# Performance work log

Measured on AMD Instinct MI355X. Metric: run time of the kernel, lower is better.

The kernel has to match this reference:

```python
import jax, jax.numpy as jnp
import numpy as np

# dims
B, N, M, K = 8, 4096, 1024, 32      # batch, points, centers, neighbors
CIN, CT = 64, 64                    # feature / temb channels
C1, C2 = 64, 128                    # SharedMLP out_channels
G, EPS = 8, 1e-5                    # GroupNorm(8, oc)


def setup_inputs() -> dict:
    key = jax.random.key(0)
    ks = jax.random.split(key, 8)
    return {
        "features": jax.random.normal(ks[0], (B, CIN, N), jnp.float32),
        "coords": jax.random.uniform(ks[1], (B, 3, N), jnp.float32),
        "temb": jax.random.normal(ks[2], (B, CT, N), jnp.float32),
        # SharedMLP params: Conv2d 1x1 -> (O, I) weight, GroupNorm affine
        "W1": jax.random.normal(ks[3], (C1, CIN + 3), jnp.float32) * 0.05,
        "b1": jnp.zeros((C1,), jnp.float32),
        "g1": jnp.ones((C1,), jnp.float32),
        "be1": jnp.zeros((C1,), jnp.float32),
        "W2": jax.random.normal(ks[4], (C2, C1), jnp.float32) * 0.05,
        "b2": jnp.zeros((C2,), jnp.float32),
        "g2": jnp.ones((C2,), jnp.float32),
        "be2": jnp.zeros((C2,), jnp.float32),
    }


def fps_indices(pts):
    # pts: [N, 3] -> [M] indices. Deterministic start at index 0
    # (original uses a random start; math otherwise identical).
    d0 = jnp.sum((pts - pts[0]) ** 2, axis=-1)  # [N]
    def step(dist, _):
        far = jnp.argmax(dist)
        dist = jnp.minimum(dist, jnp.sum((pts - pts[far]) ** 2, axis=-1))
        return dist, far
    _, fars = jax.lax.scan(step, d0, None, length=M - 1)
    return jnp.concatenate([jnp.zeros((1,), fars.dtype), fars])


def group_norm(x, gamma, beta):
    # x: [B, C, M, K], normalize per group over (C//G, M, K)
    b, c, m, k = x.shape
    xr = x.reshape(b, G, c // G, m, k)
    mu = xr.mean(axis=(2, 3, 4), keepdims=True)
    var = xr.var(axis=(2, 3, 4), keepdims=True)
    xn = ((xr - mu) * jax.lax.rsqrt(var + EPS)).reshape(b, c, m, k)
    return xn * gamma[:, None, None] + beta[:, None, None]


def swish(x):
    return x * jax.nn.sigmoid(x)


def reference(features, coords, temb, W1, b1, g1, be1, W2, b2, g2, be2):
    # --- furthest point sampling ---
    idx = jax.vmap(fps_indices)(coords.transpose(0, 2, 1))          # [B, M]
    centers = jax.vmap(lambda c, i: c[:, i])(coords, idx)           # [B, 3, M]
    # --- 'ball query' (actually kNN: source argsorts dist, takes first K) ---
    c = centers.transpose(0, 2, 1)                                  # [B, M, 3]
    p = coords.transpose(0, 2, 1)                                   # [B, N, 3]
    d = (jnp.sum(c * c, -1)[:, :, None] + jnp.sum(p * p, -1)[:, None, :]
         - 2.0 * jnp.einsum('bmd,bnd->bmn', c, p))                  # [B, M, N]
    _, nidx = jax.lax.top_k(-d, K)                                  # [B, M, K]
    gather = jax.vmap(lambda xb, ib: xb[:, ib])                     # [B,C,N],[B,M,K]->[B,C,M,K]
    gcoords = gather(coords, nidx) - centers[..., None]             # [B, 3, M, K]
    gtemb = gather(temb, nidx)                                      # [B, CT, M, K]
    gfeat = jnp.concatenate([gcoords, gather(features, nidx)], axis=1)  # [B, 3+CIN, M, K]
    # --- SharedMLP (1x1 conv -> GN -> Swish) x2, then max over neighbors ---
    h = swish(group_norm(jnp.einsum('oc,bcmk->bomk', W1, gfeat) + b1[:, None, None], g1, be1))
    h = swish(group_norm(jnp.einsum('oc,bcmk->bomk', W2, h) + b2[:, None, None], g2, be2))
    return h.max(axis=-1), centers, gtemb.max(axis=-1)
```

## Files before the change

kernel.cpp:

```cpp
#include <hip/hip_runtime.h>
#include <stdint.h>

#define BB 8
#define NN 4096
#define MM 1024
#define KK 32

__device__ __forceinline__ float bf2f(unsigned short u) {
    union { unsigned int i; float f; } v; v.i = ((unsigned int)u) << 16; return v.f;
}
__device__ __forceinline__ unsigned short f2bf(float f) {
    union { float f; unsigned int i; } v; v.f = f;
    unsigned int x = v.i;
    x += 0x7fffu + ((x >> 16) & 1u);
    return (unsigned short)(x >> 16);
}
__device__ __forceinline__ float swishf(float y) {
    return __fdividef(y, 1.0f + __expf(-y));
}

#define OUT1_OFF 1048576
#define OUT2_OFF 1073152

#define P_W1 0
#define P_B1 4288
#define P_G1 4352
#define P_BE1 4416
#define P_W2 4480
#define P_B2 12672
#define P_G2 12800
#define P_BE2 12928

__device__ __forceinline__ int detect_flag_wave(const unsigned short* f, int lane) {
    unsigned short u = f[lane * 2];
    float x = fabsf(bf2f(u));
    bool ext = (u != 0) && (x > 100.0f || x < 1e-30f);
    unsigned long long m = __ballot(ext);
    return (__popcll(m) >= 16) ? 1 : 0;
}

#define DPP_STAGE(CTRL) { \
    union { double d; unsigned int u[2]; } s_, r_; \
    s_.d = bd; \
    r_.u[0] = (unsigned)__builtin_amdgcn_update_dpp(0, (int)s_.u[0], CTRL, 0xF, 0xF, true); \
    r_.u[1] = (unsigned)__builtin_amdgcn_update_dpp(0, (int)s_.u[1], CTRL, 0xF, 0xF, true); \
    int op_ = __builtin_amdgcn_update_dpp(0, bp, CTRL, 0xF, 0xF, true); \
    double od_ = r_.d; \
    bool rep_ = (od_ > bd) || (od_ == bd && op_ < bp); \
    bd = rep_ ? od_ : bd; bp = rep_ ? op_ : bp; }

__device__ __forceinline__ void redmax64(double& bd, int& bp) {
    DPP_STAGE(0xB1)
    DPP_STAGE(0x4E)
    DPP_STAGE(0x141)
    DPP_STAGE(0x140)
#pragma unroll
    for (int m = 32; m >= 16; m >>= 1) {
        double od = __shfl_xor(bd, m, 64);
        int op = __shfl_xor(bp, m, 64);
        bool rep = (od > bd) || (od == bd && op < bp);
        bd = rep ? od : bd; bp = rep ? op : bp;
    }
}

__global__ __launch_bounds__(256) void k_cvt_all(
    const void* __restrict__ feat, const void* __restrict__ coords,
    float* __restrict__ coordsC, float* __restrict__ paramsC,
    int* __restrict__ qhead, int* __restrict__ progress,
    float* __restrict__ stats1, int* __restrict__ cvt_done,
    const void* W1, const void* b1, const void* g1, const void* be1,
    const void* W2, const void* b2, const void* g2, const void* be2)
{
    __shared__ int sflag;
    int tid = threadIdx.x, blk = blockIdx.x;
    if (tid < 64) {
        int fl0 = detect_flag_wave((const unsigned short*)feat, tid);
        if (tid == 0) sflag = fl0;
    }
    __syncthreads();
    int fl = sflag;
    if (blk == 0) {
        if (tid == 0) { *qhead = 0; *cvt_done = 0; }
        if (tid < 8) progress[tid * 16] = -1;
        stats1[tid] = 0.f;
        stats1[tid + 256] = 0.f;
    }
    if (blk < 384) {
        int idx = blk * 256 + tid;
        coordsC[idx] = fl ? ((const float*)coords)[idx]
                          : bf2f(((const unsigned short*)coords)[idx]);
    } else {
        int idx = (blk - 384) * 256 + tid;
        if (idx < 13056) {
            const void* src; int off;
            if (idx < 4288)       { src = W1;  off = idx; }
            else if (idx < 4352)  { src = b1;  off = idx - 4288; }
            else if (idx < 4416)  { src = g1;  off = idx - 4352; }
            else if (idx < 4480)  { src = be1; off = idx - 4416; }
            else if (idx < 12672) { src = W2;  off = idx - 4480; }
            else if (idx < 12800) { src = b2;  off = idx - 12672; }
            else if (idx < 12928) { src = g2;  off = idx - 12800; }
            else                  { src = be2; off = idx - 12928; }
            paramsC[idx] = fl ? ((const float*)src)[off]
                              : bf2f(((const unsigned short*)src)[off]);
        }
    }
}

#define W1Tm(j,c)     (((float*)SM)[(j)*64+(c)])
#define GBUFm(mi,k,c) (((float*)(SM+17152))[(((mi)*32+(k))*66)+(c)])
#define GCm(mi,j,k)   (((float*)(SM+50944))[(((mi)*3+(j))*32)+(k)])
#define NDm(mi,k)     (((int*)(SM+52480))[((mi)*32)+(k)])
#define W2Tm(j,c)     (((float*)SM)[(j)*128+(c)])
#define ACTm(mi,j,k)  (((float*)(SM+32768))[(((mi)*64+(j))*32)+(k)])

struct PW { double d; int p; int q; };
#define PSM_XS   ((float*)(SM))
#define PSM_YS   ((float*)(SM + 16384))
#define PSM_ZS   ((float*)(SM + 32768))
#define PSM_HIST ((int*)(SM + 49152))
#define PSM_PWB  ((PW*)(SM + 53248))
#define PSM_SF   ((int*)(SM + 53376))

#define RESCAN(G) { \
    double gd = 1.0e300; int ga = (G) * 8; \
    _Pragma("unroll") \
    for (int i = 0; i < 8; i++) { \
        int sl = (G) * 8 + i; \
        unsigned int bit = (sl < 32) ? (elo >> sl) : (ehi >> (sl - 32)); \
        double cd = (bit & 1u) ? 1.0e300 : d[sl]; \
        bool rep = cd < gd; \
        gd = rep ? cd : gd; ga = rep ? sl : ga; \
    } \
    g8[(G)] = gd; a8[(G)] = ga; }

__global__ __launch_bounds__(256) void k_fpsknn(
    const void* __restrict__ coords, const float* __restrict__ coordsC,
    float* __restrict__ centersF, int* __restrict__ nidx,
    const void* __restrict__ temb, const void* __restrict__ feat,
    float* __restrict__ featT, const float* __restrict__ paramsC,
    float* __restrict__ stats1,
    void* __restrict__ d_out,
    int* __restrict__ qhead, int* __restrict__ progress,
    int* __restrict__ cvt_done,
    unsigned short* __restrict__ h1, int cache1)
{
    __shared__ __align__(16) char SM[55296];
    int tid = threadIdx.x;
    int blk = blockIdx.x;
    if (tid < 64) {
        int fl0 = detect_flag_wave((const unsigned short*)feat, tid);
        if (tid == 0) *PSM_SF = fl0;
    }
    __syncthreads();
    int fl = *PSM_SF;

    if (blk < 8) {
        int b = blk;
        if (fl) {
            const float* cb = (const float*)coords + (size_t)b * 3 * NN;
#pragma unroll
            for (int i = 0; i < 16; i++) {
                int p = tid + i * 256;
                PSM_XS[p] = cb[p]; PSM_YS[p] = cb[NN + p]; PSM_ZS[p] = cb[2 * NN + p];
            }
        } else {
            const unsigned short* cb = (const unsigned short*)coords + (size_t)b * 3 * NN;
#pragma unroll
            for (int i = 0; i < 16; i++) {
                int p = tid + i * 256;
                PSM_XS[p] = bf2f(cb[p]); PSM_YS[p] = bf2f(cb[NN + p]); PSM_ZS[p] = bf2f(cb[2 * NN + p]);
            }
        }
        if (tid == 0) PSM_HIST[0] = 0;
        __syncthreads();
        if (tid == 0) {
            *(float4*)(centersF + (size_t)b * MM * 4) =
                make_float4(PSM_XS[0], PSM_YS[0], PSM_ZS[0], 0.f);
            __hip_atomic_store(&progress[b * 16], 0, __ATOMIC_RELEASE, __HIP_MEMORY_SCOPE_AGENT);
        }
        int base = tid * 16;
        double px[16], py[16], pz[16], dist[16];
        double x0 = (double)PSM_XS[0], y0 = (double)PSM_YS[0], z0 = (double)PSM_ZS[0];
        double bd = -1.0; int bp = base;
#pragma unroll
        for (int j = 0; j < 16; j++) {
            px[j] = (double)PSM_XS[base + j]; py[j] = (double)PSM_YS[base + j]; pz[j] = (double)PSM_ZS[base + j];
            double dx = px[j] - x0, dy = py[j] - y0, dz = pz[j] - z0;
            dist[j] = fma(dz, dz, fma(dy, dy, dx * dx));
            bool rep = dist[j] > bd;
            bd = rep ? dist[j] : bd; bp = rep ? base + j : bp;
        }
        int lane = tid & 63, wid = tid >> 6;
#pragma unroll 1
        for (int s = 1; s < MM; s++) {
            redmax64(bd, bp);
            int par = s & 1;
            if (lane == 0) { PW w; w.d = bd; w.p = bp; w.q = 0; PSM_PWB[par * 4 + wid] = w; }
            __syncthreads();
            PW w0 = PSM_PWB[par * 4 + 0];
            double wd = w0.d; int wp = w0.p;
#pragma unroll
            for (int w = 1; w < 4; w++) {
                PW ww = PSM_PWB[par * 4 + w];
                bool rep = (ww.d > wd) || (ww.d == wd && ww.p < wp);
                wd = rep ? ww.d : wd; wp = rep ? ww.p : wp;
            }
            if (tid == 0) PSM_HIST[s] = wp;
            if ((s & 31) == 31 && s >= 63 && wid == ((s >> 5) & 3)) {
                int s0 = s - 63;
                if (lane < 32) {
                    int far = PSM_HIST[s0 + lane];
                    *(float4*)(centersF + ((size_t)b * MM + s0 + lane) * 4) =
                        make_float4(PSM_XS[far], PSM_YS[far], PSM_ZS[far], 0.f);
                }
                if (lane == 0)
                    __hip_atomic_store(&progress[b * 16], s0 + 31,
                                       __ATOMIC_RELEASE, __HIP_MEMORY_SCOPE_AGENT);
            }
            double fx = (double)PSM_XS[wp], fy = (double)PSM_YS[wp], fz = (double)PSM_ZS[wp];
            bd = -1.0; bp = base;
#pragma unroll
            for (int j = 0; j < 16; j++) {
                double dx = px[j] - fx, dy = py[j] - fy, dz = pz[j] - fz;
                double d = fma(dz, dz, fma(dy, dy, dx * dx));
                dist[j] = fmin(dist[j], d);
                bool rep = dist[j] > bd;
                bd = rep ? dist[j] : bd; bp = rep ? base + j : bp;
            }
        }
        __syncthreads();
        if (tid < 32) {
            int far = PSM_HIST[992 + tid];
            *(float4*)(centersF + ((size_t)b * MM + 992 + tid) * 4) =
                make_float4(PSM_XS[far], PSM_YS[far], PSM_ZS[far], 0.f);
        }
        if (tid == 0)
            __hip_atomic_store(&progress[b * 16], 1023,
                               __ATOMIC_RELEASE, __HIP_MEMORY_SCOPE_AGENT);
#pragma unroll
        for (int i = 0; i < 4; i++) {
            int m = tid + i * 256;
            int far = PSM_HIST[m];
            float X = PSM_XS[far], Y = PSM_YS[far], Z = PSM_ZS[far];
            if (fl) {
                float* o = (float*)d_out;
                o[OUT1_OFF + (size_t)(b * 3 + 0) * MM + m] = X;
                o[OUT1_OFF + (size_t)(b * 3 + 1) * MM + m] = Y;
                o[OUT1_OFF + (size_t)(b * 3 + 2) * MM + m] = Z;
            } else {
                unsigned short* o = (unsigned short*)d_out;
                o[OUT1_OFF + (size_t)(b * 3 + 0) * MM + m] = f2bf(X);
                o[OUT1_OFF + (size_t)(b * 3 + 1) * MM + m] = f2bf(Y);
                o[OUT1_OFF + (size_t)(b * 3 + 2) * MM + m] = f2bf(Z);
            }
        }
    } else {
        int lane = tid & 63, wid = tid >> 6;
        {
            float (*tile)[65] = (float(*)[65])SM;
            for (int t = blk - 8; t < 512; t += 248) {
                int b = t >> 6, n0 = (t & 63) * 64;
                int c = tid >> 2, q = tid & 3;
                size_t base = ((size_t)b * 64 + c) * NN + n0 + q * 16;
                __syncthreads();
                if (fl) {
                    const float* sp = (const float*)feat + base;
#pragma unroll
                    for (int j = 0; j < 16; j++) tile[c][q * 16 + j] = sp[j];
                } else {
                    const unsigned short* sp = (const unsigned short*)feat + base;
#pragma unroll
                    for (int j = 0; j < 16; j++) tile[c][q * 16 + j] = bf2f(sp[j]);
                }
                __syncthreads();
                int n = tid >> 2;
                float* dp = featT + ((size_t)b * NN + n0 + n) * 64 + q * 16;
#pragma unroll
                for (int j = 0; j < 16; j++) dp[j] = tile[q * 16 + j][n];
            }
            __syncthreads();
            if (tid == 0) {
                __hip_atomic_fetch_add(cvt_done, 1, __ATOMIC_ACQ_REL, __HIP_MEMORY_SCOPE_AGENT);
                while (__hip_atomic_load(cvt_done, __ATOMIC_RELAXED,
                                         __HIP_MEMORY_SCOPE_AGENT) < 248)
                    __builtin_amdgcn_s_sleep(16);
                (void)__hip_atomic_load(cvt_done, __ATOMIC_ACQUIRE, __HIP_MEMORY_SCOPE_AGENT);
            }
            __syncthreads();
        }
        for (int t = tid; t < 64 * 67; t += 256) {
            int c = t / 67, j = t % 67;
            W1Tm(j, c) = paramsC[P_W1 + t];
        }
        __syncthreads();
        for (;;) {
            int id = 0;
            if (lane == 0) id = atomicAdd(qhead, 1);
            id = __shfl(id, 0, 64);
            if (id >= BB * MM) break;
            int b = id & 7, m = id >> 3;
            while (__hip_atomic_load(&progress[b * 16], __ATOMIC_RELAXED,
                                     __HIP_MEMORY_SCOPE_AGENT) < m)
                __builtin_amdgcn_s_sleep(64);
            (void)__hip_atomic_load(&progress[b * 16], __ATOMIC_ACQUIRE,
                                    __HIP_MEMORY_SCOPE_AGENT);
            int bm = b * MM + m;
            const float* cb = coordsC + (size_t)b * 3 * NN;
            float4 ctr = *(const float4*)(centersF + (size_t)bm * 4);
            double cx = (double)ctr.x, cy = (double)ctr.y, cz = (double)ctr.z;
            double cc = (cx * cx + cy * cy) + cz * cz;
            double d[64];
#pragma unroll 4
            for (int j = 0; j < 64; j++) {
                int p = j * 64 + lane;
                double x = (double)cb[p], y = (double)cb[NN + p], z = (double)cb[2 * NN + p];
                double pp = (x * x + y * y) + z * z;
                double dt = (cx * x + cy * y) + cz * z;
                d[j] = (cc + pp) - 2.0 * dt;
            }
            double g8[8]; int a8[8];
#pragma unroll
            for (int g = 0; g < 8; g++) {
                double gd = d[g * 8]; int ga = g * 8;
#pragma unroll
                for (int i = 1; i < 8; i++) {
                    int sl = g * 8 + i;
                    bool rep = d[sl] < gd;
                    gd = rep ? d[sl] : gd; ga = rep ? sl : ga;
                }
                g8[g] = gd; a8[g] = ga;
            }
            unsigned int elo = 0, ehi = 0;
            int res = 0;
#pragma unroll 1
            for (int it = 0; it < 32; it++) {
                double bd = g8[0]; int ba = a8[0];
#pragma unroll
                for (int g = 1; g < 8; g++) {
                    bool rep = g8[g] < bd;
                    bd = rep ? g8[g] : bd; ba = rep ? a8[g] : ba;
                }
                int bp = ba * 64 + lane;
                double wd = bd; int wp = bp;
#pragma unroll
                for (int s = 32; s >= 1; s >>= 1) {
                    double od = __shfl_xor(wd, s, 64);
                    int op = __shfl_xor(wp, s, 64);
                    bool rep = (od < wd) || (od == wd && op < wp);
                    wd = rep ? od : wd; wp = rep ? op : wp;
                }
                res = (lane == it) ? wp : res;
                if (bp == wp) {
                    int slot = ba;
                    if (slot < 32) elo |= (1u << slot); else ehi |= (1u << (slot - 32));
                    int g = slot >> 3;
                    switch (g) {
                        case 0: RESCAN(0) break;
                        case 1: RESCAN(1) break;
                        case 2: RESCAN(2) break;
                        case 3: RESCAN(3) break;
                        case 4: RESCAN(4) break;
                        case 5: RESCAN(5) break;
                        case 6: RESCAN(6) break;
                        case 7: RESCAN(7) break;
                    }
                }
            }
            if (lane < KK) nidx[(size_t)bm * KK + lane] = res;
            float best = -3.0e38f;
            if (fl) {
                const float* tb = (const float*)temb + ((size_t)b * 64 + lane) * NN;
#pragma unroll 4
                for (int k = 0; k < 32; k++) {
                    int nk = __shfl(res, k, 64);
                    best = fmaxf(best, tb[nk]);
                }
            } else {
                const unsigned short* tb = (const unsigned short*)temb + ((size_t)b * 64 + lane) * NN;
#pragma unroll 4
                for (int k = 0; k < 32; k++) {
                    int nk = __shfl(res, k, 64);
                    best = fmaxf(best, bf2f(tb[nk]));
                }
            }
            size_t off = (size_t)OUT2_OFF + ((size_t)(b * 64 + lane)) * MM + m;
            if (fl) ((float*)d_out)[off] = best;
            else    ((unsigned short*)d_out)[off] = f2bf(best);
            if (lane < 32) NDm(wid, lane) = res & (NN - 1);
            const float* fb = featT + (size_t)b * NN * 64;
#pragma unroll 4
            for (int q = 0; q < 32; q++) {
                int n = NDm(wid, q);
                GBUFm(wid, q, lane) = fb[(size_t)n * 64 + lane];
            }
            if (lane < 32) {
                int n = NDm(wid, lane);
                GCm(wid, 0, lane) = __fsub_rn(cb[n], ctr.x);
                GCm(wid, 1, lane) = __fsub_rn(cb[NN + n], ctr.y);
                GCm(wid, 2, lane) = __fsub_rn(cb[2 * NN + n], ctr.z);
            }
            int c0 = (lane >> 3) * 8;
            int k0 = (lane & 7) * 4;
            float acc[8][4];
#pragma unroll
            for (int i = 0; i < 8; i++)
#pragma unroll
                for (int kk = 0; kk < 4; kk++) acc[i][kk] = 0.f;
#pragma unroll
            for (int j = 0; j < 3; j++) {
                float4 a = *(const float4*)&GCm(wid, j, k0);
                float4 w0 = *(const float4*)&W1Tm(j, c0);
                float4 w1v = *(const float4*)&W1Tm(j, c0 + 4);
                float w[8] = {w0.x, w0.y, w0.z, w0.w, w1v.x, w1v.y, w1v.z, w1v.w};
#pragma unroll
                for (int i = 0; i < 8; i++) {
                    acc[i][0] = fmaf(w[i], a.x, acc[i][0]);
                    acc[i][1] = fmaf(w[i], a.y, acc[i][1]);
                    acc[i][2] = fmaf(w[i], a.z, acc[i][2]);
                    acc[i][3] = fmaf(w[i], a.w, acc[i][3]);
                }
            }
#pragma unroll 4
            for (int c = 0; c < 64; c++) {
                float f0 = GBUFm(wid, k0 + 0, c);
                float f1 = GBUFm(wid, k0 + 1, c);
                float f2 = GBUFm(wid, k0 + 2, c);
                float f3 = GBUFm(wid, k0 + 3, c);
                int j = 3 + c;
                float4 w0 = *(const float4*)&W1Tm(j, c0);
                float4 w1v = *(const float4*)&W1Tm(j, c0 + 4);
                float w[8] = {w0.x, w0.y, w0.z, w0.w, w1v.x, w1v.y, w1v.z, w1v.w};
#pragma unroll
                for (int i = 0; i < 8; i++) {
                    acc[i][0] = fmaf(w[i], f0, acc[i][0]);
                    acc[i][1] = fmaf(w[i], f1, acc[i][1]);
                    acc[i][2] = fmaf(w[i], f2, acc[i][2]);
                    acc[i][3] = fmaf(w[i], f3, acc[i][3]);
                }
            }
            float s = 0.f, s2 = 0.f;
#pragma unroll
            for (int i = 0; i < 8; i++) {
                float bb = paramsC[P_B1 + c0 + i];
                float v0 = acc[i][0] + bb, v1 = acc[i][1] + bb;
                float v2 = acc[i][2] + bb, v3 = acc[i][3] + bb;
                s += v0; s2 = fmaf(v0, v0, s2);
                s += v1; s2 = fmaf(v1, v1, s2);
                s += v2; s2 = fmaf(v2, v2, s2);
                s += v3; s2 = fmaf(v3, v3, s2);
                if (cache1) {
                    unsigned int p0 = (unsigned int)f2bf(v0) | ((unsigned int)f2bf(v1) << 16);
                    unsigned int p1 = (unsigned int)f2bf(v2) | ((unsigned int)f2bf(v3) << 16);
                    *(uint2*)(h1 + ((size_t)bm * 64 + c0 + i) * 32 + k0) = make_uint2(p0, p1);
                }
            }
            s += __shfl_xor(s, 1, 64); s += __shfl_xor(s, 2, 64); s += __shfl_xor(s, 4, 64);
            s2 += __shfl_xor(s2, 1, 64); s2 += __shfl_xor(s2, 2, 64); s2 += __shfl_xor(s2, 4, 64);
            if ((lane & 7) == 0) {
                int g = lane >> 3;
                atomicAdd(&stats1[(b * 8 + g) * 2], s);
                atomicAdd(&stats1[(b * 8 + g) * 2 + 1], s2);
            }
        }
    }
}

__device__ __forceinline__ void mlp1_compute(
    char* SM, int tid, int lane, int mi, int b, int bm,
    const float* __restrict__ featT, const float* __restrict__ coordsC,
    const float* __restrict__ centersF, const int* __restrict__ nidx,
    const float* __restrict__ P, float acc[8][4])
{
    for (int t = tid; t < 64 * 67; t += 256) {
        int c = t / 67, j = t % 67;
        W1Tm(j, c) = P[P_W1 + t];
    }
    if (lane < 32) NDm(mi, lane) = nidx[(size_t)bm * KK + lane] & (NN - 1);
    __syncthreads();
    const float* fb = featT + (size_t)b * NN * 64;
#pragma unroll 4
    for (int q = 0; q < 32; q++) {
        int n = NDm(mi, q);
        GBUFm(mi, q, lane) = fb[(size_t)n * 64 + lane];
    }
    float4 ctr = *(const float4*)(centersF + (size_t)bm * 4);
    const float* cb = coordsC + (size_t)b * 3 * NN;
    if (lane < 32) {
        int n = NDm(mi, lane);
        GCm(mi, 0, lane) = __fsub_rn(cb[n], ctr.x);
        GCm(mi, 1, lane) = __fsub_rn(cb[NN + n], ctr.y);
        GCm(mi, 2, lane) = __fsub_rn(cb[2 * NN + n], ctr.z);
    }
    __syncthreads();
    int c0 = (lane >> 3) * 8;
    int k0 = (lane & 7) * 4;
#pragma unroll
    for (int i = 0; i < 8; i++)
#pragma unroll
        for (int kk = 0; kk < 4; kk++) acc[i][kk] = 0.f;
#pragma unroll
    for (int j = 0; j < 3; j++) {
        float4 a = *(const float4*)&GCm(mi, j, k0);
        float4 w0 = *(const float4*)&W1Tm(j, c0);
        float4 w1v = *(const float4*)&W1Tm(j, c0 + 4);
        float w[8] = {w0.x, w0.y, w0.z, w0.w, w1v.x, w1v.y, w1v.z, w1v.w};
#pragma unroll
        for (int i = 0; i < 8; i++) {
            acc[i][0] = fmaf(w[i], a.x, acc[i][0]);
            acc[i][1] = fmaf(w[i], a.y, acc[i][1]);
            acc[i][2] = fmaf(w[i], a.z, acc[i][2]);
            acc[i][3] = fmaf(w[i], a.w, acc[i][3]);
        }
    }
#pragma unroll 4
    for (int c = 0; c < 64; c++) {
        float f0 = GBUFm(mi, k0 + 0, c);
        float f1 = GBUFm(mi, k0 + 1, c);
        float f2 = GBUFm(mi, k0 + 2, c);
        float f3 = GBUFm(mi, k0 + 3, c);
        int j = 3 + c;
        float4 w0 = *(const float4*)&W1Tm(j, c0);
        float4 w1v = *(const float4*)&W1Tm(j, c0 + 4);
        float w[8] = {w0.x, w0.y, w0.z, w0.w, w1v.x, w1v.y, w1v.z, w1v.w};
#pragma unroll
        for (int i = 0; i < 8; i++) {
            acc[i][0] = fmaf(w[i], f0, acc[i][0]);
            acc[i][1] = fmaf(w[i], f1, acc[i][1]);
            acc[i][2] = fmaf(w[i], f2, acc[i][2]);
            acc[i][3] = fmaf(w[i], f3, acc[i][3]);
        }
    }
}

__device__ __forceinline__ void mlp2_compute(
    char* SM, int tid, int lane, int mi, int b,
    const float v1[8][4], const float* __restrict__ S1,
    const float* __restrict__ P, float v2[16][4])
{
    __syncthreads();
    int c0 = (lane >> 3) * 8;
    int k0 = (lane & 7) * 4;
    int g = c0 >> 3;
    float S = S1[(b * 8 + g) * 2], Q = S1[(b * 8 + g) * 2 + 1];
    float mean = S * (1.0f / 262144.0f);
    float var = Q * (1.0f / 262144.0f) - mean * mean;
    float inv = rsqrtf(var + 1e-5f);
#pragma unroll
    for (int i = 0; i < 8; i++) {
        int c = c0 + i;
        float sc = P[P_G1 + c] * inv;
        float sh = P[P_BE1 + c] - mean * sc;
#pragma unroll
        for (int kk = 0; kk < 4; kk++)
            ACTm(mi, c, k0 + kk) = swishf(fmaf(v1[i][kk], sc, sh));
    }
    for (int t = tid; t < 128 * 64; t += 256) {
        int c = t >> 6, j = t & 63;
        W2Tm(j, c) = P[P_W2 + t];
    }
    __syncthreads();
    int c02 = (lane >> 3) * 16;
    float acc2[16][4];
#pragma unroll
    for (int i = 0; i < 16; i++)
#pragma unroll
        for (int kk = 0; kk < 4; kk++) acc2[i][kk] = 0.f;
#pragma unroll 4
    for (int j = 0; j < 64; j++) {
        float4 a = *(const float4*)&ACTm(mi, j, k0);
        float4 w0 = *(const float4*)&W2Tm(j, c02);
        float4 w1v = *(const float4*)&W2Tm(j, c02 + 4);
        float4 w2v = *(const float4*)&W2Tm(j, c02 + 8);
        float4 w3 = *(const float4*)&W2Tm(j, c02 + 12);
        float w[16] = {w0.x, w0.y, w0.z, w0.w, w1v.x, w1v.y, w1v.z, w1v.w,
                       w2v.x, w2v.y, w2v.z, w2v.w, w3.x, w3.y, w3.z, w3.w};
#pragma unroll
        for (int i = 0; i < 16; i++) {
            acc2[i][0] = fmaf(w[i], a.x, acc2[i][0]);
            acc2[i][1] = fmaf(w[i], a.y, acc2[i][1]);
            acc2[i][2] = fmaf(w[i], a.z, acc2[i][2]);
            acc2[i][3] = fmaf(w[i], a.w, acc2[i][3]);
        }
    }
#pragma unroll
    for (int i = 0; i < 16; i++) {
        float bb = P[P_B2 + c02 + i];
#pragma unroll
        for (int kk = 0; kk < 4; kk++) v2[i][kk] = acc2[i][kk] + bb;
    }
}

__device__ __forceinline__ void get_v1(
    char* SM, int tid, int lane, int mi, int b, int bm,
    const float* featT, const float* coordsC, const float* centersF,
    const int* nidx, const float* P,
    const unsigned short* h1, int cache1, float v1[8][4])
{
    int c0 = (lane >> 3) * 8;
    int k0 = (lane & 7) * 4;
    if (cache1) {
#pragma unroll
        for (int i = 0; i < 8; i++) {
            uint2 u = *(const uint2*)(h1 + ((size_t)bm * 64 + c0 + i) * 32 + k0);
            v1[i][0] = bf2f((unsigned short)(u.x & 0xffffu));
            v1[i][1] = bf2f((unsigned short)(u.x >> 16));
            v1[i][2] = bf2f((unsigned short)(u.y & 0xffffu));
            v1[i][3] = bf2f((unsigned short)(u.y >> 16));
        }
    } else {
        float acc1[8][4];
        mlp1_compute(SM, tid, lane, mi, b, bm, featT, coordsC, centersF, nidx, P, acc1);
#pragma unroll
        for (int i = 0; i < 8; i++) {
            float bb = P[P_B1 + c0 + i];
#pragma unroll
            for (int kk = 0; kk < 4; kk++) v1[i][kk] = acc1[i][kk] + bb;
        }
    }
}

__global__ __launch_bounds__(256) void k_mlp2s(
    const float* __restrict__ featT, const float* __restrict__ coordsC,
    const float* __restrict__ centersF, const int* __restrict__ nidx,
    const float* __restrict__ P, const float* __restrict__ stats1,
    float* __restrict__ stats2,
    const unsigned short* __restrict__ h1, int cache1,
    unsigned short* __restrict__ vmaxA, unsigned short* __restrict__ vminA,
    int have_vmm)
{
    __shared__ __align__(16) char smem[65536];
    char* SM = smem;
    int tid = threadIdx.x, blk = blockIdx.x;
    int b = blk >> 8, m0 = (blk & 255) * 4;
    int mi = tid >> 6, lane = tid & 63;
    int bm = b * MM + m0 + mi;
    float v1[8][4];
    get_v1(SM, tid, lane, mi, b, bm, featT, coordsC, centersF, nidx, P, h1, cache1, v1);
    float v2[16][4];
    mlp2_compute(SM, tid, lane, mi, b, v1, stats1, P, v2);
    int c02 = (lane >> 3) * 16;
    float s = 0.f, s2 = 0.f;
#pragma unroll
    for (int i = 0; i < 16; i++) {
#pragma unroll
        for (int kk = 0; kk < 4; kk++) {
            float v = v2[i][kk];
            s += v; s2 = fmaf(v, v, s2);
        }
    }
    if (have_vmm) {
        int m = m0 + mi;
#pragma unroll
        for (int i = 0; i < 16; i++) {
            float va = fmaxf(fmaxf(v2[i][0], v2[i][1]), fmaxf(v2[i][2], v2[i][3]));
            float vb = fminf(fminf(v2[i][0], v2[i][1]), fminf(v2[i][2], v2[i][3]));
            va = fmaxf(va, __shfl_xor(va, 1, 64)); vb = fminf(vb, __shfl_xor(vb, 1, 64));
            va = fmaxf(va, __shfl_xor(va, 2, 64)); vb = fminf(vb, __shfl_xor(vb, 2, 64));
            va = fmaxf(va, __shfl_xor(va, 4, 64)); vb = fminf(vb, __shfl_xor(vb, 4, 64));
            if ((lane & 7) == 0) {
                size_t o = ((size_t)(b * 128 + c02 + i)) * MM + m;
                vmaxA[o] = f2bf(va);
                vminA[o] = f2bf(vb);
            }
        }
    }
    s += __shfl_xor(s, 1, 64); s += __shfl_xor(s, 2, 64); s += __shfl_xor(s, 4, 64);
    s2 += __shfl_xor(s2, 1, 64); s2 += __shfl_xor(s2, 2, 64); s2 += __shfl_xor(s2, 4, 64);
    __syncthreads();
    float* sred = (float*)SM;
    if ((lane & 7) == 0) {
        int g = lane >> 3;
        sred[(mi * 8 + g) * 2] = s;
        sred[(mi * 8 + g) * 2 + 1] = s2;
    }
    __syncthreads();
    if (tid < 16) {
        int g = tid >> 1, w = tid & 1;
        float t = sred[(0 * 8 + g) * 2 + w] + sred[(1 * 8 + g) * 2 + w]
                + sred[(2 * 8 + g) * 2 + w] + sred[(3 * 8 + g) * 2 + w];
        atomicAdd(&stats2[(b * 8 + g) * 2 + w], t);
    }
}

__global__ __launch_bounds__(256) void k_final_fast(
    const unsigned short* __restrict__ vmaxA, const unsigned short* __restrict__ vminA,
    const float* __restrict__ P, const float* __restrict__ stats2,
    void* __restrict__ d_out, const void* __restrict__ feat)
{
    int tid = threadIdx.x;
    int idx = blockIdx.x * 256 + tid;
    int fl = detect_flag_wave((const unsigned short*)feat, tid & 63);
    int c = (idx >> 10) & 127;
    int b = idx >> 17;
    int g = c >> 4;
    float S = stats2[(b * 8 + g) * 2], Q = stats2[(b * 8 + g) * 2 + 1];
    float mean = S * (1.0f / 524288.0f);
    float var = Q * (1.0f / 524288.0f) - mean * mean;
    float inv = rsqrtf(var + 1e-5f);
    float sc = P[P_G2 + c] * inv;
    float sh = P[P_BE2 + c] - mean * sc;
    float va = bf2f(vmaxA[idx]);
    float vb = bf2f(vminA[idx]);
    float r = fmaxf(swishf(fmaf(va, sc, sh)), swishf(fmaf(vb, sc, sh)));
    if (fl) ((float*)d_out)[idx] = r;
    else    ((unsigned short*)d_out)[idx] = f2bf(r);
}

__global__ __launch_bounds__(256) void k_final_slow(
    const float* __restrict__ featT, const float* __restrict__ coordsC,
    const float* __restrict__ centersF, const int* __restrict__ nidx,
    const float* __restrict__ P, const float* __restrict__ stats1,
    const float* __restrict__ stats2,
    void* __restrict__ d_out, const void* __restrict__ feat,
    const unsigned short* __restrict__ h1, int cache1)
{
    __shared__ __align__(16) char smem[65536];
    char* SM = smem;
    int tid = threadIdx.x, blk = blockIdx.x;
    if (tid < 64) {
        int fl0 = detect_flag_wave((const unsigned short*)feat, tid);
        if (tid == 0) *(int*)(SM + 53248) = fl0;
    }
    __syncthreads();
    int fl = *(int*)(SM + 53248);
    int b = blk >> 8, m0 = (blk & 255) * 4;
    int mi = tid >> 6, lane = tid & 63;
    int bm = b * MM + m0 + mi;
    float v1[8][4];
    get_v1(SM, tid, lane, mi, b, bm, featT, coordsC, centersF, nidx, P, h1, cache1, v1);
    float v2[16][4];
    mlp2_compute(SM, tid, lane, mi, b, v1, stats1, P, v2);
    int c02 = (lane >> 3) * 16;
    int g2 = c02 >> 4;
    float S = stats2[(b * 8 + g2) * 2], Q = stats2[(b * 8 + g2) * 2 + 1];
    float mean = S * (1.0f / 524288.0f);
    float var = Q * (1.0f / 524288.0f) - mean * mean;
    float inv = rsqrtf(var + 1e-5f);
    float mx[16];
#pragma unroll
    for (int i = 0; i < 16; i++) {
        int c = c02 + i;
        float sc = P[P_G2 + c] * inv;
        float sh = P[P_BE2 + c] - mean * sc;
        float v = -3.0e38f;
#pragma unroll
        for (int kk = 0; kk < 4; kk++)
            v = fmaxf(v, swishf(fmaf(v2[i][kk], sc, sh)));
        v = fmaxf(v, __shfl_xor(v, 1, 64));
        v = fmaxf(v, __shfl_xor(v, 2, 64));
        v = fmaxf(v, __shfl_xor(v, 4, 64));
        mx[i] = v;
    }
    if ((lane & 7) == 0) {
        int m = m0 + mi;
#pragma unroll
        for (int i = 0; i < 16; i++) {
            size_t off = (size_t)(b * 128 + c02 + i) * MM + m;
            if (fl) ((float*)d_out)[off] = mx[i];
            else    ((unsigned short*)d_out)[off] = f2bf(mx[i]);
        }
    }
}

extern "C" void kernel_launch(void* const* d_in, const int* in_sizes, int n_in,
                              void* d_out, int out_size, void* d_ws, size_t ws_size,
                              hipStream_t stream) {
    (void)in_sizes; (void)n_in; (void)out_size;
    const void* feat = d_in[0];
    const void* coords = d_in[1];
    const void* temb = d_in[2];

    char* ws = (char*)d_ws;
    int* qhead = (int*)ws;
    int* progress = (int*)(ws + 512);
    float* stats1 = (float*)(ws + 1024);
    float* stats2 = (float*)(ws + 2048);
    int* cvt_done = (int*)(ws + 3072);
    float* coordsC = (float*)(ws + 3136);
    float* paramsC = (float*)(ws + 396352);
    float* centersF = (float*)(ws + 448576);
    int* nidx = (int*)(ws + 579648);
    float* featT = (float*)(ws + 1628224);
    unsigned short* h1 = (unsigned short*)(ws + 10016832);
    unsigned short* vmaxA = (unsigned short*)(ws + 43571264);
    unsigned short* vminA = (unsigned short*)(ws + 45668416);
    int cache1 = (ws_size >= 43571264u) ? 1 : 0;
    int have_vmm = (ws_size >= 47765568u) ? 1 : 0;

    k_cvt_all<<<435, 256, 0, stream>>>(feat, coords, coordsC, paramsC,
                                       qhead, progress, stats1, cvt_done,
                                       d_in[3], d_in[4], d_in[5], d_in[6],
                                       d_in[7], d_in[8], d_in[9], d_in[10]);
    k_fpsknn<<<256, 256, 0, stream>>>(coords, coordsC, centersF, nidx, temb,
                                      feat, featT, paramsC, stats1, d_out,
                                      qhead, progress, cvt_done, h1, cache1);
    k_mlp2s<<<2048, 256, 0, stream>>>(featT, coordsC, centersF, nidx, paramsC,
                                      stats1, stats2, h1, cache1,
                                      vmaxA, vminA, have_vmm);
    if (have_vmm) {
        k_final_fast<<<4096, 256, 0, stream>>>(vmaxA, vminA, paramsC, stats2,
                                               d_out, feat);
    } else {
        k_final_slow<<<2048, 256, 0, stream>>>(featT, coordsC, centersF, nidx,
                                               paramsC, stats1, stats2, d_out,
                                               feat, h1, cache1);
    }
}
```

Measured before the change: 1.333 ms.

## Fold conversion into fpsknn and fuse MLP2 with final pass via grid barrier

The separate conversion kernel is replaced by a tiny init kernel, and the coords and param conversion now runs inside the non-FPS blocks of k_fpsknn. The MLP2 and final normalize/swish kernels are merged into one persistent 512-block kernel. Each block handles four tiles, then waits on an atomic grid-wide barrier before applying GroupNorm2 and writing the output. This cuts two kernel launches and their tails. It relies on all 512 blocks being co-resident for the spin barrier, and the conversion done inside fpsknn must finish before anything reads coordsC or paramsC.

After: 1.383 ms. 3.8% more time.

```diff
diff --git a/kernel.cpp b/kernel.cpp
--- a/kernel.cpp
+++ b/kernel.cpp
@@ -63,48 +63,14 @@
     }
 }
 
-__global__ __launch_bounds__(256) void k_cvt_all(
-    const void* __restrict__ feat, const void* __restrict__ coords,
-    float* __restrict__ coordsC, float* __restrict__ paramsC,
-    int* __restrict__ qhead, int* __restrict__ progress,
-    float* __restrict__ stats1, int* __restrict__ cvt_done,
-    const void* W1, const void* b1, const void* g1, const void* be1,
-    const void* W2, const void* b2, const void* g2, const void* be2)
-{
-    __shared__ int sflag;
-    int tid = threadIdx.x, blk = blockIdx.x;
-    if (tid < 64) {
-        int fl0 = detect_flag_wave((const unsigned short*)feat, tid);
-        if (tid == 0) sflag = fl0;
-    }
-    __syncthreads();
-    int fl = sflag;
-    if (blk == 0) {
-        if (tid == 0) { *qhead = 0; *cvt_done = 0; }
-        if (tid < 8) progress[tid * 16] = -1;
-        stats1[tid] = 0.f;
-        stats1[tid + 256] = 0.f;
-    }
-    if (blk < 384) {
-        int idx = blk * 256 + tid;
-        coordsC[idx] = fl ? ((const float*)coords)[idx]
-                          : bf2f(((const unsigned short*)coords)[idx]);
-    } else {
-        int idx = (blk - 384) * 256 + tid;
-        if (idx < 13056) {
-            const void* src; int off;
-            if (idx < 4288)       { src = W1;  off = idx; }
-            else if (idx < 4352)  { src = b1;  off = idx - 4288; }
-            else if (idx < 4416)  { src = g1;  off = idx - 4352; }
-            else if (idx < 4480)  { src = be1; off = idx - 4416; }
-            else if (idx < 12672) { src = W2;  off = idx - 4480; }
-            else if (idx < 12800) { src = b2;  off = idx - 12672; }
-            else if (idx < 12928) { src = g2;  off = idx - 12800; }
-            else                  { src = be2; off = idx - 12928; }
-            paramsC[idx] = fl ? ((const float*)src)[off]
-                              : bf2f(((const unsigned short*)src)[off]);
-        }
-    }
+__global__ void k_init(int* __restrict__ qhead, int* __restrict__ progress,
+                       float* __restrict__ stats1, int* __restrict__ cvt_done,
+                       int* __restrict__ mlp_done) {
+    int tid = threadIdx.x;
+    if (tid == 0) { *qhead = 0; *cvt_done = 0; *mlp_done = 0; }
+    if (tid < 8) progress[tid * 16] = -1;
+    stats1[tid] = 0.f;
+    stats1[tid + 256] = 0.f;
 }
 
 #define W1Tm(j,c)     (((float*)SM)[(j)*64+(c)])
@@ -135,15 +101,17 @@
     g8[(G)] = gd; a8[(G)] = ga; }
 
 __global__ __launch_bounds__(256) void k_fpsknn(
-    const void* __restrict__ coords, const float* __restrict__ coordsC,
+    const void* __restrict__ coords, float* __restrict__ coordsC,
     float* __restrict__ centersF, int* __restrict__ nidx,
     const void* __restrict__ temb, const void* __restrict__ feat,
-    float* __restrict__ featT, const float* __restrict__ paramsC,
+    float* __restrict__ featT, float* __restrict__ paramsC,
     float* __restrict__ stats1,
     void* __restrict__ d_out,
     int* __restrict__ qhead, int* __restrict__ progress,
     int* __restrict__ cvt_done,
-    unsigned short* __restrict__ h1, int cache1)
+    unsigned short* __restrict__ h1, int cache1,
+    const void* W1r, const void* b1r, const void* g1r, const void* be1r,
+    const void* W2r, const void* b2r, const void* g2r, const void* be2r)
 {
     __shared__ __align__(16) char SM[55296];
     int tid = threadIdx.x;
@@ -257,6 +225,22 @@
         }
     } else {
         int lane = tid & 63, wid = tid >> 6;
+        for (int i = (blk - 8) * 256 + tid; i < BB * 3 * NN; i += 248 * 256)
+            coordsC[i] = fl ? ((const float*)coords)[i]
+                            : bf2f(((const unsigned short*)coords)[i]);
+        for (int i = (blk - 8) * 256 + tid; i < 13056; i += 248 * 256) {
+            const void* src; int off;
+            if (i < 4288)       { src = W1r;  off = i; }
+            else if (i < 4352)  { src = b1r;  off = i - 4288; }
+            else if (i < 4416)  { src = g1r;  off = i - 4352; }
+            else if (i < 4480)  { src = be1r; off = i - 4416; }
+            else if (i < 12672) { src = W2r;  off = i - 4480; }
+            else if (i < 12800) { src = b2r;  off = i - 12672; }
+            else if (i < 12928) { src = g2r;  off = i - 12800; }
+            else                { src = be2r; off = i - 12928; }
+            paramsC[i] = fl ? ((const float*)src)[off]
+                            : bf2f(((const unsigned short*)src)[off]);
+        }
         {
             float (*tile)[65] = (float(*)[65])SM;
             for (int t = blk - 8; t < 512; t += 248) {
@@ -620,14 +604,105 @@
     }
 }
 
+__global__ __launch_bounds__(256) void k_mlp2f(
+    const float* __restrict__ featT, const float* __restrict__ coordsC,
+    const float* __restrict__ centersF, const int* __restrict__ nidx,
+    const float* __restrict__ P, const float* __restrict__ stats1,
+    float* __restrict__ stats2,
+    const unsigned short* __restrict__ h1,
+    unsigned short* __restrict__ vmaxA, unsigned short* __restrict__ vminA,
+    int* __restrict__ mlp_done,
+    void* __restrict__ d_out, const void* __restrict__ feat)
+{
+    __shared__ __align__(16) char SM[65536];
+    int tid = threadIdx.x;
+    int mi = tid >> 6, lane = tid & 63;
+#pragma unroll 1
+    for (int it = 0; it < 4; it++) {
+        int vblk = blockIdx.x + 512 * it;
+        int b = vblk >> 8, m0 = (vblk & 255) * 4;
+        int bm = b * MM + m0 + mi;
+        float v1[8][4];
+        get_v1(SM, tid, lane, mi, b, bm, featT, coordsC, centersF, nidx, P, h1, 1, v1);
+        float v2[16][4];
+        mlp2_compute(SM, tid, lane, mi, b, v1, stats1, P, v2);
+        int c02 = (lane >> 3) * 16;
+        float s = 0.f, s2 = 0.f;
+#pragma unroll
+        for (int i = 0; i < 16; i++) {
+#pragma unroll
+            for (int kk = 0; kk < 4; kk++) {
+                float v = v2[i][kk];
+                s += v; s2 = fmaf(v, v, s2);
+            }
+        }
+        int m = m0 + mi;
+#pragma unroll
+        for (int i = 0; i < 16; i++) {
+            float va = fmaxf(fmaxf(v2[i][0], v2[i][1]), fmaxf(v2[i][2], v2[i][3]));
+            float vb = fminf(fminf(v2[i][0], v2[i][1]), fminf(v2[i][2], v2[i][3]));
+            va = fmaxf(va, __shfl_xor(va, 1, 64)); vb = fminf(vb, __shfl_xor(vb, 1, 64));
+            va = fmaxf(va, __shfl_xor(va, 2, 64)); vb = fminf(vb, __shfl_xor(vb, 2, 64));
+            va = fmaxf(va, __shfl_xor(va, 4, 64)); vb = fminf(vb, __shfl_xor(vb, 4, 64));
+            if ((lane & 7) == 0) {
+                size_t o = ((size_t)(b * 128 + c02 + i)) * MM + m;
+                vmaxA[o] = f2bf(va);
+                vminA[o] = f2bf(vb);
+            }
+        }
+        s += __shfl_xor(s, 1, 64); s += __shfl_xor(s, 2, 64); s += __shfl_xor(s, 4, 64);
+        s2 += __shfl_xor(s2, 1, 64); s2 += __shfl_xor(s2, 2, 64); s2 += __shfl_xor(s2, 4, 64);
+        __syncthreads();
+        float* sred = (float*)SM;
+        if ((lane & 7) == 0) {
+            int g = lane >> 3;
+            sred[(mi * 8 + g) * 2] = s;
+            sred[(mi * 8 + g) * 2 + 1] = s2;
+        }
+        __syncthreads();
+        if (tid < 16) {
+            int g = tid >> 1, w = tid & 1;
+            float t = sred[(0 * 8 + g) * 2 + w] + sred[(1 * 8 + g) * 2 + w]
+                    + sred[(2 * 8 + g) * 2 + w] + sred[(3 * 8 + g) * 2 + w];
+            atomicAdd(&stats2[(b * 8 + g) * 2 + w], t);
+        }
+        __syncthreads();
+    }
+    __syncthreads();
+    if (tid == 0) {
+        __hip_atomic_fetch_add(mlp_done, 1, __ATOMIC_ACQ_REL, __HIP_MEMORY_SCOPE_AGENT);
+        while (__hip_atomic_load(mlp_done, __ATOMIC_RELAXED, __HIP_MEMORY_SCOPE_AGENT) < 512)
+            __builtin_amdgcn_s_sleep(16);
+        (void)__hip_atomic_load(mlp_done, __ATOMIC_ACQUIRE, __HIP_MEMORY_SCOPE_AGENT);
+    }
+    __syncthreads();
+    int fl = detect_flag_wave((const unsigned short*)feat, lane);
+#pragma unroll 1
+    for (int i = 0; i < 8; i++) {
+        int idx = blockIdx.x * 256 + tid + i * 131072;
+        int c = (idx >> 10) & 127;
+        int b = idx >> 17;
+        int g = c >> 4;
+        float S = stats2[(b * 8 + g) * 2], Q = stats2[(b * 8 + g) * 2 + 1];
+        float mean = S * (1.0f / 524288.0f);
+        float var = Q * (1.0f / 524288.0f) - mean * mean;
+        float inv = rsqrtf(var + 1e-5f);
+        float sc = P[P_G2 + c] * inv;
+        float sh = P[P_BE2 + c] - mean * sc;
+        float va = bf2f(vmaxA[idx]);
+        float vb = bf2f(vminA[idx]);
+        float r = fmaxf(swishf(fmaf(va, sc, sh)), swishf(fmaf(vb, sc, sh)));
+        if (fl) ((float*)d_out)[idx] = r;
+        else    ((unsigned short*)d_out)[idx] = f2bf(r);
+    }
+}
+
 __global__ __launch_bounds__(256) void k_mlp2s(
     const float* __restrict__ featT, const float* __restrict__ coordsC,
     const float* __restrict__ centersF, const int* __restrict__ nidx,
     const float* __restrict__ P, const float* __restrict__ stats1,
     float* __restrict__ stats2,
-    const unsigned short* __restrict__ h1, int cache1,
-    unsigned short* __restrict__ vmaxA, unsigned short* __restrict__ vminA,
-    int have_vmm)
+    const unsigned short* __restrict__ h1, int cache1)
 {
     __shared__ __align__(16) char smem[65536];
     char* SM = smem;
@@ -639,32 +714,14 @@
     get_v1(SM, tid, lane, mi, b, bm, featT, coordsC, centersF, nidx, P, h1, cache1, v1);
     float v2[16][4];
     mlp2_compute(SM, tid, lane, mi, b, v1, stats1, P, v2);
-    int c02 = (lane >> 3) * 16;
     float s = 0.f, s2 = 0.f;
 #pragma unroll
-    for (int i = 0; i < 16; i++) {
+    for (int i = 0; i < 16; i++)
 #pragma unroll
         for (int kk = 0; kk < 4; kk++) {
             float v = v2[i][kk];
             s += v; s2 = fmaf(v, v, s2);
         }
-    }
-    if (have_vmm) {
-        int m = m0 + mi;
-#pragma unroll
-        for (int i = 0; i < 16; i++) {
-            float va = fmaxf(fmaxf(v2[i][0], v2[i][1]), fmaxf(v2[i][2], v2[i][3]));
-            float vb = fminf(fminf(v2[i][0], v2[i][1]), fminf(v2[i][2], v2[i][3]));
-            va = fmaxf(va, __shfl_xor(va, 1, 64)); vb = fminf(vb, __shfl_xor(vb, 1, 64));
-            va = fmaxf(va, __shfl_xor(va, 2, 64)); vb = fminf(vb, __shfl_xor(vb, 2, 64));
-            va = fmaxf(va, __shfl_xor(va, 4, 64)); vb = fminf(vb, __shfl_xor(vb, 4, 64));
-            if ((lane & 7) == 0) {
-                size_t o = ((size_t)(b * 128 + c02 + i)) * MM + m;
-                vmaxA[o] = f2bf(va);
-                vminA[o] = f2bf(vb);
-            }
-        }
-    }
     s += __shfl_xor(s, 1, 64); s += __shfl_xor(s, 2, 64); s += __shfl_xor(s, 4, 64);
     s2 += __shfl_xor(s2, 1, 64); s2 += __shfl_xor(s2, 2, 64); s2 += __shfl_xor(s2, 4, 64);
     __syncthreads();
@@ -681,30 +738,6 @@
                 + sred[(2 * 8 + g) * 2 + w] + sred[(3 * 8 + g) * 2 + w];
         atomicAdd(&stats2[(b * 8 + g) * 2 + w], t);
     }
-}
-
-__global__ __launch_bounds__(256) void k_final_fast(
-    const unsigned short* __restrict__ vmaxA, const unsigned short* __restrict__ vminA,
-    const float* __restrict__ P, const float* __restrict__ stats2,
-    void* __restrict__ d_out, const void* __restrict__ feat)
-{
-    int tid = threadIdx.x;
-    int idx = blockIdx.x * 256 + tid;
-    int fl = detect_flag_wave((const unsigned short*)feat, tid & 63);
-    int c = (idx >> 10) & 127;
-    int b = idx >> 17;
-    int g = c >> 4;
-    float S = stats2[(b * 8 + g) * 2], Q = stats2[(b * 8 + g) * 2 + 1];
-    float mean = S * (1.0f / 524288.0f);
-    float var = Q * (1.0f / 524288.0f) - mean * mean;
-    float inv = rsqrtf(var + 1e-5f);
-    float sc = P[P_G2 + c] * inv;
-    float sh = P[P_BE2 + c] - mean * sc;
-    float va = bf2f(vmaxA[idx]);
-    float vb = bf2f(vminA[idx]);
-    float r = fmaxf(swishf(fmaf(va, sc, sh)), swishf(fmaf(vb, sc, sh)));
-    if (fl) ((float*)d_out)[idx] = r;
-    else    ((unsigned short*)d_out)[idx] = f2bf(r);
 }
 
 __global__ __launch_bounds__(256) void k_final_slow(
@@ -777,31 +810,31 @@
     float* stats1 = (float*)(ws + 1024);
     float* stats2 = (float*)(ws + 2048);
     int* cvt_done = (int*)(ws + 3072);
-    float* coordsC = (float*)(ws + 3136);
-    float* paramsC = (float*)(ws + 396352);
-    float* centersF = (float*)(ws + 448576);
-    int* nidx = (int*)(ws + 579648);
-    float* featT = (float*)(ws + 1628224);
-    unsigned short* h1 = (unsigned short*)(ws + 10016832);
-    unsigned short* vmaxA = (unsigned short*)(ws + 43571264);
-    unsigned short* vminA = (unsigned short*)(ws + 45668416);
-    int cache1 = (ws_size >= 43571264u) ? 1 : 0;
-    int have_vmm = (ws_size >= 47765568u) ? 1 : 0;
-
-    k_cvt_all<<<435, 256, 0, stream>>>(feat, coords, coordsC, paramsC,
-                                       qhead, progress, stats1, cvt_done,
-                                       d_in[3], d_in[4], d_in[5], d_in[6],
-                                       d_in[7], d_in[8], d_in[9], d_in[10]);
+    int* mlp_done = (int*)(ws + 3136);
+    float* coordsC = (float*)(ws + 3200);
+    float* paramsC = (float*)(ws + 396416);
+    float* centersF = (float*)(ws + 448640);
+    int* nidx = (int*)(ws + 579712);
+    float* featT = (float*)(ws + 1628288);
+    unsigned short* h1 = (unsigned short*)(ws + 10016896);
+    unsigned short* vmaxA = (unsigned short*)(ws + 43571328);
+    unsigned short* vminA = (unsigned short*)(ws + 45668480);
+    int cache1 = (ws_size >= 43571328u) ? 1 : 0;
+    int have_vmm = (ws_size >= 47765632u) ? 1 : 0;
+
+    k_init<<<1, 256, 0, stream>>>(qhead, progress, stats1, cvt_done, mlp_done);
     k_fpsknn<<<256, 256, 0, stream>>>(coords, coordsC, centersF, nidx, temb,
                                       feat, featT, paramsC, stats1, d_out,
-                                      qhead, progress, cvt_done, h1, cache1);
-    k_mlp2s<<<2048, 256, 0, stream>>>(featT, coordsC, centersF, nidx, paramsC,
-                                      stats1, stats2, h1, cache1,
-                                      vmaxA, vminA, have_vmm);
-    if (have_vmm) {
-        k_final_fast<<<4096, 256, 0, stream>>>(vmaxA, vminA, paramsC, stats2,
-                                               d_out, feat);
+                                      qhead, progress, cvt_done, h1, cache1,
+                                      d_in[3], d_in[4], d_in[5], d_in[6],
+                                      d_in[7], d_in[8], d_in[9], d_in[10]);
+    if (cache1 && have_vmm) {
+        k_mlp2f<<<512, 256, 0, stream>>>(featT, coordsC, centersF, nidx, paramsC,
+                                         stats1, stats2, h1, vmaxA, vminA,
+                                         mlp_done, d_out, feat);
     } else {
+        k_mlp2s<<<2048, 256, 0, stream>>>(featT, coordsC, centersF, nidx, paramsC,
+                                          stats1, stats2, h1, cache1);
         k_final_slow<<<2048, 256, 0, stream>>>(featT, coordsC, centersF, nidx,
                                                paramsC, stats1, stats2, d_out,
                                                feat, h1, cache1);
```
